# Kernel optimization log

Hardware: AMD Instinct MI355X
Metric: run time of the kernel (lower is better)

Reference implementation:

```python
import jax, jax.numpy as jnp
import numpy as np

CONF_THRES = 0.4
IOU_THRES = 0.45
MAX_WH = 4096.0   # class offset for class-aware NMS (agnostic=False)
MAX_DET = 300
B, N, NC = 8, 25200, 80


def setup_inputs() -> dict:
    key = jax.random.key(0)
    k1, k2, k3, k4, k5 = jax.random.split(key, 5)
    # realistic raw detector output: xywh in pixels, obj/cls scores in [0,1]
    xy = jax.random.uniform(k1, (B, N, 2), minval=0.0, maxval=608.0)
    wh = jax.random.uniform(k2, (B, N, 2), minval=4.0, maxval=96.0)
    obj = jax.random.uniform(k3, (B, N, 1))
    cls = jax.random.uniform(k4, (B, N, NC))
    prediction = jnp.concatenate([xy, wh, obj, cls], axis=-1)  # [B,N,85]
    logits = jax.random.normal(k5, (B, N, NC))
    return {"prediction": prediction, "logits": logits}


def _xywh2xyxy(b):
    cx, cy, w, h = b[..., 0], b[..., 1], b[..., 2], b[..., 3]
    return jnp.stack([cx - w / 2, cy - h / 2, cx + w / 2, cy + h / 2], axis=-1)


def _iou_one_vs_all(box, boxes):
    # box [4], boxes [N,4] -> IoU [N]
    lt = jnp.maximum(box[:2], boxes[:, :2])
    rb = jnp.minimum(box[2:], boxes[:, 2:])
    wh = jnp.clip(rb - lt, 0.0)
    inter = wh[:, 0] * wh[:, 1]
    a1 = (box[2] - box[0]) * (box[3] - box[1])
    a2 = (boxes[:, 2] - boxes[:, 0]) * (boxes[:, 3] - boxes[:, 1])
    return inter / (a1 + a2 - inter + 1e-9)


def _nms_image(pred, log_):
    # pred [N, 5+NC], log_ [N, NC]
    obj = pred[:, 4]
    scores_all = pred[:, 5:] * obj[:, None]          # x[:,5:] *= x[:,4:5]
    conf = scores_all.max(-1)                        # best-class conf
    cls = jnp.argmax(scores_all, -1)
    # obj-conf prefilter (xc mask) AND final conf filter, expressed as masking
    valid = (obj > CONF_THRES) & (conf > CONF_THRES)
    box = _xywh2xyxy(pred[:, :4])                    # [N,4]
    obox = box + (cls.astype(box.dtype) * MAX_WH)[:, None]  # class offset
    score0 = jnp.where(valid, conf, -1.0)

    def step(score_cur, _):
        idx = jnp.argmax(score_cur)
        keep = score_cur[idx] > 0.0
        iou = _iou_one_vs_all(obox[idx], obox)
        # suppress everything with IoU > thr (includes the picked box itself)
        new_score = jnp.where(keep & (iou > IOU_THRES), -1.0, score_cur)
        return new_score, (idx, keep)

    _, (idxs, keeps) = jax.lax.scan(step, score0, None, length=MAX_DET)
    m = keeps.astype(box.dtype)[:, None]
    dets = jnp.concatenate(
        [box[idxs], conf[idxs, None], cls[idxs, None].astype(box.dtype)], axis=-1
    ) * m                                            # [MAX_DET, 6], zero-padded
    return dets, log_[idxs] * m, keeps


def reference(prediction, logits):
    # returns (dets [B,300,6] = xyxy,conf,cls ; logits_sel [B,300,80] ; keep mask [B,300])
    return jax.vmap(_nms_image)(prediction, logits)
```

## Files before the change

kernel.cpp:

```cpp
#include <hip/hip_runtime.h>

#pragma clang fp contract(off)

#define NB 8
#define NN 25200
#define NCLS 80
#define NSTR 85
#define MAXDET 300
#define CONF_T 0.4f
#define IOU_T 0.45f
#define MAX_WH_C 4096.0f

#define NBIN 1024
#define BINSHIFT 14
#define BINBASE 0x3EC00000u
#define SELN 512
#define SORTN 2048
#define PREP_ROWS 64

typedef unsigned long long ull;

__device__ __forceinline__ float cand_score(const float* __restrict__ p) {
    float obj = p[4];
    float best = p[5] * obj;
    for (int j = 1; j < NCLS; ++j) {
        float s = p[5 + j] * obj;
        if (s > best) best = s;
    }
    return ((obj > CONF_T) && (best > CONF_T)) ? best : -1.0f;
}
__device__ __forceinline__ int cand_cls(const float* __restrict__ p) {
    float obj = p[4];
    float best = p[5] * obj; int bc = 0;
    for (int j = 1; j < NCLS; ++j) {
        float s = p[5 + j] * obj;
        if (s > best) { best = s; bc = j; }
    }
    return bc;
}
__device__ __forceinline__ bool iou_gt(float ax1, float ay1, float ax2, float ay2, float aarea,
                                       float bx1, float by1, float bx2, float by2, float barea) {
    float lx = fmaxf(ax1, bx1);
    float ly = fmaxf(ay1, by1);
    float rx = fminf(ax2, bx2);
    float ry = fminf(ay2, by2);
    float iw = fmaxf(rx - lx, 0.0f);
    float ih = fmaxf(ry - ly, 0.0f);
    float inter = iw * ih;
    float iou = inter / ((aarea + barea - inter) + 1e-9f);
    return iou > IOU_T;
}

__global__ __launch_bounds__(256) void prep_kernel(const float* __restrict__ pred,
                                                   float* __restrict__ score_ws,
                                                   int* __restrict__ cls_ws,
                                                   int write_cls) {
    __shared__ float st[PREP_ROWS * NSTR];
    const int R0 = blockIdx.x * PREP_ROWS;
    const float4* src = reinterpret_cast<const float4*>(pred + (size_t)R0 * NSTR);
    float4* dst4 = reinterpret_cast<float4*>(st);
    const int tid = threadIdx.x;
    for (int i = tid; i < PREP_ROWS * NSTR / 4; i += 256) dst4[i] = src[i];
    __syncthreads();

    int row = tid >> 2, part = tid & 3;
    const float* pr = st + row * NSTR;
    float obj = pr[4];
    float best = -1.0f; int bc = part * 20;
    const float* pc = pr + 5 + part * 20;
#pragma unroll
    for (int k = 0; k < 20; ++k) {
        float s = pc[k] * obj;
        if (s > best) { best = s; bc = part * 20 + k; }
    }
#pragma unroll
    for (int d = 1; d <= 2; d <<= 1) {
        float ob = __shfl_xor(best, d);
        int   oc = __shfl_xor(bc, d);
        if (ob > best || (ob == best && oc < bc)) { best = ob; bc = oc; }
    }
    if (part == 0) {
        int grow = R0 + row;
        bool valid = (obj > CONF_T) && (best > CONF_T);
        score_ws[grow] = valid ? best : -1.0f;
        if (write_cls) cls_ws[grow] = bc;
    }
}

__global__ __launch_bounds__(1024) void selimg_kernel(const float* __restrict__ pred,
                                                      const float* __restrict__ score_ws,
                                                      const int* __restrict__ cls_ws, int use_cls,
                                                      int* __restrict__ cnt_ws, int* __restrict__ total_ws,
                                                      ull* __restrict__ sel_key,
                                                      float* __restrict__ sel_x1, float* __restrict__ sel_y1,
                                                      float* __restrict__ sel_x2, float* __restrict__ sel_y2,
                                                      float* __restrict__ sel_area, float* __restrict__ sel_cls,
                                                      int* __restrict__ sel_idx) {
    __shared__ int s_hist[NBIN];
    __shared__ ull s_key[SELN];
    __shared__ int s_gidx[SELN];
    __shared__ int s_cnt, s_T, s_total;
    const int b = blockIdx.x;
    const int tid = threadIdx.x;
    const int lane = tid & 63;
    const int wid = tid >> 6;
    const float* predb = pred + (size_t)b * NN * NSTR;
    const float* sb = score_ws + (size_t)b * NN;

    s_hist[tid] = 0;
    if (tid == 0) s_cnt = 0;
    __syncthreads();
    for (int g = tid; g < NN; g += 1024) {
        float s = sb[g];
        if (s > 0.0f) {
            int bin = (int)((__float_as_uint(s) - BINBASE) >> BINSHIFT);
            atomicAdd(&s_hist[bin], 1);
        }
    }
    __syncthreads();
    if (wid == 0) {
        int acc = 0; int S[16];
#pragma unroll
        for (int k = 15; k >= 0; --k) { acc += s_hist[lane * 16 + k]; S[k] = acc; }
        int tot = acc;
        int incl = tot;
#pragma unroll
        for (int d = 1; d < 64; d <<= 1) {
            int v = __shfl_down(incl, d);
            if (lane + d < 64) incl += v;
        }
        int E = incl - tot;
        int Tl = NBIN;
#pragma unroll
        for (int k = 0; k < 16; ++k)
            if (Tl == NBIN && S[k] + E <= SELN) Tl = lane * 16 + k;
        int total0 = incl;
#pragma unroll
        for (int d = 1; d < 64; d <<= 1) {
            int o = __shfl_xor(Tl, d);
            if (o < Tl) Tl = o;
        }
        if (lane == 0) { s_T = Tl; s_total = total0; }
    }
    __syncthreads();
    int T = s_T;
    for (int g = tid; g < NN; g += 1024) {
        float s = sb[g];
        if (s > 0.0f) {
            int bin = (int)((__float_as_uint(s) - BINBASE) >> BINSHIFT);
            if (bin >= T) {
                int pos = atomicAdd(&s_cnt, 1);
                if (pos < SELN) {
                    s_key[pos] = ((ull)__float_as_uint(s) << 32)
                                 | (unsigned int)(0xFFFFFFFFu - (unsigned int)g);
                    s_gidx[pos] = g;
                }
            }
        }
    }
    __syncthreads();
    int cnt = s_cnt; if (cnt > SELN) cnt = SELN;

    if (tid < cnt) {
        int g = s_gidx[tid];
        const float* p = predb + (size_t)g * NSTR;
        float cx = p[0], cy = p[1], w = p[2], h = p[3];
        int c = use_cls ? cls_ws[(size_t)b * NN + g] : cand_cls(p);
        float off = (float)c * MAX_WH_C;
        float x1 = (cx - w * 0.5f) + off;
        float y1 = (cy - h * 0.5f) + off;
        float x2 = (cx + w * 0.5f) + off;
        float y2 = (cy + h * 0.5f) + off;
        int o = b * SELN + tid;
        sel_key[o] = s_key[tid];
        sel_x1[o] = x1; sel_y1[o] = y1; sel_x2[o] = x2; sel_y2[o] = y2;
        sel_area[o] = (x2 - x1) * (y2 - y1);
        sel_cls[o] = (float)c;
        sel_idx[o] = g;
    }
    if (tid == 0) { cnt_ws[b] = cnt; total_ws[b] = s_total; }
}

__global__ __launch_bounds__(256) void mask_kernel(const int* __restrict__ cnt_ws,
                                                   const ull* __restrict__ sel_key,
                                                   const float* __restrict__ sel_x1, const float* __restrict__ sel_y1,
                                                   const float* __restrict__ sel_x2, const float* __restrict__ sel_y2,
                                                   const float* __restrict__ sel_area,
                                                   ull* __restrict__ mask_ws) {
    __shared__ ull skey[SELN];
    __shared__ float ox1[SELN], oy1[SELN], ox2[SELN], oy2[SELN], oar[SELN];
    const int b = blockIdx.x >> 4;
    const int chunk = blockIdx.x & 15;
    const int tid = threadIdx.x;
    int cnt = cnt_ws[b]; if (cnt > SELN) cnt = SELN;
    for (int s = tid; s < SELN; s += 256) {
        if (s < cnt) {
            skey[s] = sel_key[b * SELN + s];
            ox1[s] = sel_x1[b * SELN + s]; oy1[s] = sel_y1[b * SELN + s];
            ox2[s] = sel_x2[b * SELN + s]; oy2[s] = sel_y2[b * SELN + s];
            oar[s] = sel_area[b * SELN + s];
        } else skey[s] = 0ull;
    }
    __syncthreads();
    int i = chunk * 32 + (tid & 31);
    int w = tid >> 5;
    if (i < cnt) {
        ull ki = skey[i];
        float ax1 = ox1[i], ay1 = oy1[i], ax2 = ox2[i], ay2 = oy2[i], aar = oar[i];
        ull m = 0ull;
        int jb = w << 6;
        int jend = cnt - jb; if (jend > 64) jend = 64;
        for (int t = 0; t < jend; ++t) {
            int j = jb + t;
            bool s = (skey[j] > ki) && iou_gt(ax1, ay1, ax2, ay2, aar,
                                             ox1[j], oy1[j], ox2[j], oy2[j], oar[j]);
            m |= (ull)s << t;
        }
        mask_ws[b * (8 * SELN) + w * SELN + i] = m;
    }
}

__global__ __launch_bounds__(1024) void resolve_kernel(
        const float* __restrict__ pred, const float* __restrict__ logits,
        const float* __restrict__ score_ws, const int* __restrict__ cls_ws, int use_cls,
        const int* __restrict__ cnt_ws, const int* __restrict__ total_ws,
        const ull* __restrict__ mask_ws, const ull* __restrict__ sel_key,
        const float* __restrict__ sel_x1, const float* __restrict__ sel_y1,
        const float* __restrict__ sel_x2, const float* __restrict__ sel_y2,
        const float* __restrict__ sel_area, const float* __restrict__ sel_cls,
        const int* __restrict__ sel_idx,
        float* __restrict__ out) {
    __shared__ ull s_m[8][SELN];
    __shared__ ull s_key[SELN];
    __shared__ ull s_kw[8];
    __shared__ ull s_minkey;
    __shared__ float s_x1[SELN], s_y1[SELN], s_x2[SELN], s_y2[SELN], s_ar[SELN], s_cl[SELN];
    __shared__ int s_ix[SELN];
    __shared__ float kx1[MAXDET], ky1[MAXDET], kx2[MAXDET], ky2[MAXDET], kar[MAXDET];
    __shared__ float ksc[MAXDET], kcl[MAXDET];
    __shared__ int kix[MAXDET];
    __shared__ int s_kc;

    const int b = blockIdx.x;
    const int tid = threadIdx.x;
    const int lane = tid & 63;
    const int wid = tid >> 6;
    const float* predb = pred + (size_t)b * NN * NSTR;
    const float* logb  = logits + (size_t)b * NN * NCLS;
    const float* sb    = score_ws + (size_t)b * NN;

    int cnt = cnt_ws[b]; if (cnt > SELN) cnt = SELN;

    for (int i = tid; i < 8 * SELN; i += 1024)
        (&s_m[0][0])[i] = mask_ws[b * (8 * SELN) + i];
    for (int s = tid; s < SELN; s += 1024) {
        if (s < cnt) {
            s_key[s] = sel_key[b * SELN + s];
            s_x1[s] = sel_x1[b * SELN + s]; s_y1[s] = sel_y1[b * SELN + s];
            s_x2[s] = sel_x2[b * SELN + s]; s_y2[s] = sel_y2[b * SELN + s];
            s_ar[s] = sel_area[b * SELN + s]; s_cl[s] = sel_cls[b * SELN + s];
            s_ix[s] = sel_idx[b * SELN + s];
        } else s_key[s] = 0ull;
    }
    __syncthreads();

    if (wid == 0) {
        ull mk = ~0ull;
#pragma unroll
        for (int r = 0; r < 8; ++r) {
            int i = (r << 6) + lane;
            if (i < cnt) { ull k = s_key[i]; if (k < mk) mk = k; }
        }
#pragma unroll
        for (int d = 32; d >= 1; d >>= 1) {
            ull o = __shfl_xor(mk, d);
            if (o < mk) mk = o;
        }
        if (lane == 0) s_minkey = mk;

        ull vm[8], kw[8];
#pragma unroll
        for (int r = 0; r < 8; ++r) {
            int lo = r << 6;
            vm[r] = (cnt >= lo + 64) ? ~0ull : (cnt > lo ? ((1ull << (cnt - lo)) - 1ull) : 0ull);
            kw[r] = vm[r];
        }
        for (int round = 0; round < SELN; ++round) {
            ull nw[8];
#pragma unroll
            for (int r = 0; r < 8; ++r) {
                int i = (r << 6) + lane;
                ull supp = 0ull;
#pragma unroll
                for (int w = 0; w < 8; ++w) supp |= kw[w] & s_m[w][i];
                nw[r] = __ballot((int)(supp == 0ull)) & vm[r];
            }
            bool changed = false;
#pragma unroll
            for (int r = 0; r < 8; ++r) { changed |= (nw[r] != kw[r]); kw[r] = nw[r]; }
            if (!changed) break;
        }
        int totkept = 0;
#pragma unroll
        for (int r = 0; r < 8; ++r) totkept += __popcll(kw[r]);
        if (lane == 0) s_kc = totkept < MAXDET ? totkept : MAXDET;
        if (lane < 8) s_kw[lane] = kw[lane];
    }
    __syncthreads();
    int kc = s_kc;

    if (tid < SELN) {
        bool kept = (s_kw[tid >> 6] >> (tid & 63)) & 1ull;
        if (!kept) s_key[tid] = 0ull;
    }
    __syncthreads();

    {
        int i = tid >> 1, half = tid & 1;
        ull k = s_key[i];
        int r = 0;
        if (k != 0ull) {
            int jb = half << 8;
            for (int jj = 0; jj < 256; ++jj) {
                ull kj = s_key[jb + jj];
                r += (int)(kj > k);
            }
        }
        r += __shfl_xor(r, 1);
        if (half == 0 && k != 0ull && r < MAXDET) {
            kx1[r] = s_x1[i]; ky1[r] = s_y1[i]; kx2[r] = s_x2[i]; ky2[r] = s_y2[i];
            kar[r] = s_ar[i]; ksc[r] = __uint_as_float((unsigned int)(k >> 32));
            kcl[r] = s_cl[i]; kix[r] = s_ix[i];
        }
    }
    __syncthreads();

    if (wid == 0 && kc < MAXDET && total_ws[b] > cnt) {
        ull prevkey = (cnt > 0) ? s_minkey : ~0ull;
        while (kc < MAXDET) {
            ull best = 0ull;
            for (int i0 = lane; i0 < NN; i0 += 64) {
                float s = sb[i0];
                if (s > 0.0f) {
                    ull key = ((ull)__float_as_uint(s) << 32)
                              | (unsigned int)(0xFFFFFFFFu - (unsigned int)i0);
                    if (key < prevkey && key > best) best = key;
                }
            }
#pragma unroll
            for (int d = 32; d >= 1; d >>= 1) {
                ull o = __shfl_xor(best, d);
                if (o > best) best = o;
            }
            if (best == 0ull) break;
            prevkey = best;
            int gi = (int)(0xFFFFFFFFu - (unsigned int)(best & 0xFFFFFFFFull));
            float sc = __uint_as_float((unsigned int)(best >> 32));
            const float* pp = predb + (size_t)gi * NSTR;
            float cx = pp[0], cy = pp[1], w = pp[2], h = pp[3];
            int c = use_cls ? cls_ws[(size_t)b * NN + gi] : cand_cls(pp);
            float off = (float)c * MAX_WH_C;
            float x1 = (cx - w * 0.5f) + off;
            float y1 = (cy - h * 0.5f) + off;
            float x2 = (cx + w * 0.5f) + off;
            float y2 = (cy + h * 0.5f) + off;
            float ar = (x2 - x1) * (y2 - y1);
            bool f = false;
            for (int t = lane; t < kc; t += 64)
                if (iou_gt(kx1[t], ky1[t], kx2[t], ky2[t], kar[t], x1, y1, x2, y2, ar)) f = true;
            if (!__any((int)f)) {
                if (lane == 0) {
                    kx1[kc] = x1; ky1[kc] = y1; kx2[kc] = x2; ky2[kc] = y2;
                    kar[kc] = ar; ksc[kc] = sc; kcl[kc] = (float)c; kix[kc] = gi;
                }
                kc++;
            }
        }
        if (lane == 0) s_kc = kc;
    }
    __syncthreads();
    kc = s_kc;

    if (tid < MAXDET) {
        int t = tid;
        float o0 = 0, o1 = 0, o2 = 0, o3 = 0, o4 = 0, o5 = 0;
        if (t < kc) {
            int idx = kix[t];
            const float* pp = predb + (size_t)idx * NSTR;
            float cx = pp[0], cy = pp[1], w = pp[2], h = pp[3];
            o0 = cx - w * 0.5f; o1 = cy - h * 0.5f;
            o2 = cx + w * 0.5f; o3 = cy + h * 0.5f;
            o4 = ksc[t];        o5 = kcl[t];
        }
        float* dd = out + (size_t)b * (MAXDET * 6) + (size_t)t * 6;
        dd[0] = o0; dd[1] = o1; dd[2] = o2; dd[3] = o3; dd[4] = o4; dd[5] = o5;
        out[(size_t)NB * MAXDET * 6 + (size_t)NB * MAXDET * NCLS + (size_t)b * MAXDET + t] =
            (t < kc) ? 1.0f : 0.0f;
    }
    float* lbase = out + (size_t)NB * MAXDET * 6 + (size_t)b * (MAXDET * NCLS);
    for (int t = wid; t < MAXDET; t += 16) {
        float* dst = lbase + (size_t)t * NCLS;
        if (t < kc) {
            const float* src = logb + (size_t)kix[t] * NCLS;
            for (int c = lane; c < NCLS; c += 64) dst[c] = src[c];
        } else {
            for (int c = lane; c < NCLS; c += 64) dst[c] = 0.0f;
        }
    }
}

__global__ __launch_bounds__(1024) void fallback_kernel(const float* __restrict__ pred,
                                                        const float* __restrict__ logits,
                                                        float* __restrict__ out) {
    __shared__ ull s_keys[SORTN];
    __shared__ float sel_x1[SORTN], sel_y1[SORTN], sel_x2[SORTN], sel_y2[SORTN];
    __shared__ float sel_area[SORTN], sel_cls[SORTN];
    __shared__ int   sel_idx[SORTN];
    __shared__ float kx1[MAXDET], ky1[MAXDET], kx2[MAXDET], ky2[MAXDET], karea[MAXDET];
    __shared__ float kscore[MAXDET], kcls[MAXDET];
    __shared__ int   kidx[MAXDET];
    __shared__ int   s_hist[NBIN];
    __shared__ int   s_suppk[64];
    __shared__ unsigned int s_supmask[64][2];
    __shared__ int   s_kc, s_T, s_cnt;

    const int b = blockIdx.x;
    const int tid = threadIdx.x;
    const int lane = tid & 63;
    const int wid = tid >> 6;
    const float* predb = pred + (size_t)b * NN * NSTR;
    const float* logb  = logits + (size_t)b * NN * NCLS;

    int kc_total = 0;
    int prevT = NBIN;

    while (kc_total < MAXDET && prevT > 0) {
        s_hist[tid] = 0;
        if (tid == 0) { s_cnt = 0; s_T = NBIN; }
        __syncthreads();
        for (int i = tid; i < NN; i += 1024) {
            float s = cand_score(predb + (size_t)i * NSTR);
            if (s > 0.0f) {
                int bin = (int)((__float_as_uint(s) - BINBASE) >> BINSHIFT);
                if (bin < prevT) atomicAdd(&s_hist[bin], 1);
            }
        }
        __syncthreads();
        for (int d = 1; d < NBIN; d <<= 1) {
            int v = s_hist[tid] + ((tid + d < NBIN) ? s_hist[tid + d] : 0);
            __syncthreads();
            s_hist[tid] = v;
            __syncthreads();
        }
        if (s_hist[tid] <= SORTN) atomicMin(&s_T, tid);
        __syncthreads();
        int T = s_T;
        int rem_total = s_hist[0];
        if (T >= prevT) {
            if (rem_total == 0) { prevT = 0; break; }
            T = prevT - 1;
        }
        __syncthreads();
        for (int i = tid; i < NN; i += 1024) {
            float s = cand_score(predb + (size_t)i * NSTR);
            if (s > 0.0f) {
                int bin = (int)((__float_as_uint(s) - BINBASE) >> BINSHIFT);
                if (bin >= T && bin < prevT) {
                    int pos = atomicAdd(&s_cnt, 1);
                    if (pos < SORTN)
                        s_keys[pos] = ((ull)__float_as_uint(s) << 32)
                                      | (unsigned int)(0xFFFFFFFFu - (unsigned int)i);
                }
            }
        }
        __syncthreads();
        int cnt = s_cnt; if (cnt > SORTN) cnt = SORTN;
        int npow = 64; while (npow < cnt) npow <<= 1;
        for (int i = cnt + tid; i < npow; i += 1024) s_keys[i] = 0ull;
        __syncthreads();
        for (int k = 2; k <= npow; k <<= 1) {
            for (int j = k >> 1; j > 0; j >>= 1) {
                for (int idx = tid; idx < npow; idx += 1024) {
                    int p = idx ^ j;
                    if (p > idx) {
                        ull a = s_keys[idx], c = s_keys[p];
                        bool desc = ((idx & k) == 0);
                        if (desc ? (a < c) : (a > c)) { s_keys[idx] = c; s_keys[p] = a; }
                    }
                }
                __syncthreads();
            }
        }
        for (int t = tid; t < cnt; t += 1024) {
            ull key = s_keys[t];
            int i = (int)(0xFFFFFFFFu - (unsigned int)(key & 0xFFFFFFFFull));
            const float* p = predb + (size_t)i * NSTR;
            float cx = p[0], cy = p[1], w = p[2], h = p[3];
            int c = cand_cls(p);
            float off = (float)c * MAX_WH_C;
            float x1 = (cx - w * 0.5f) + off;
            float y1 = (cy - h * 0.5f) + off;
            float x2 = (cx + w * 0.5f) + off;
            float y2 = (cy + h * 0.5f) + off;
            sel_x1[t] = x1; sel_y1[t] = y1; sel_x2[t] = x2; sel_y2[t] = y2;
            sel_area[t] = (x2 - x1) * (y2 - y1);
            sel_cls[t] = (float)c;
            sel_idx[t] = i;
        }
        __syncthreads();
        int nb2 = (cnt + 63) >> 6;
        for (int batch = 0; batch < nb2; ++batch) {
            int kcb = kc_total;
            if (kcb >= MAXDET) break;
            if (tid < 64) { s_suppk[tid] = 0; s_supmask[tid][0] = 0u; s_supmask[tid][1] = 0u; }
            __syncthreads();
            int cloc = tid >> 4, ch = tid & 15;
            int gi = batch * 64 + cloc;
            bool validc = gi < cnt;
            float ax1 = 0, ay1 = 0, ax2 = 0, ay2 = 0, aar = 0;
            if (validc) {
                ax1 = sel_x1[gi]; ay1 = sel_y1[gi];
                ax2 = sel_x2[gi]; ay2 = sel_y2[gi]; aar = sel_area[gi];
            }
            bool flag = false;
            if (validc) {
                for (int t = ch; t < kcb; t += 16) {
                    if (iou_gt(kx1[t], ky1[t], kx2[t], ky2[t], karea[t],
                               ax1, ay1, ax2, ay2, aar)) flag = true;
                }
            }
            ull bal = __ballot((int)flag);
            if ((lane & 15) == 0) {
                unsigned int sub = (unsigned int)((bal >> (lane & 48)) & 0xFFFFull);
                s_suppk[cloc] = (sub != 0u);
            }
            unsigned int mbits = 0;
            if (validc) {
                for (int jj = 0; jj < 4; ++jj) {
                    int j = (ch << 2) + jj;
                    int gj = batch * 64 + j;
                    if (j > cloc && gj < cnt) {
                        if (iou_gt(ax1, ay1, ax2, ay2, aar,
                                   sel_x1[gj], sel_y1[gj], sel_x2[gj], sel_y2[gj], sel_area[gj]))
                            mbits |= 1u << (j & 31);
                    }
                }
            }
            if (mbits) atomicOr(&s_supmask[cloc][(ch >> 3) & 1], mbits);
            __syncthreads();
            if (wid == 0) {
                ull mask = ((ull)s_supmask[lane][1] << 32) | s_supmask[lane][0];
                bool validj = (batch * 64 + lane) < cnt;
                ull rem = __ballot((int)(validj && (s_suppk[lane] == 0)));
                ull keepbits = 0;
                int kcount = kcb;
                while (rem && kcount < MAXDET) {
                    int i = __builtin_ctzll(rem);
                    rem &= rem - 1;
                    keepbits |= 1ull << i;
                    ++kcount;
                    ull mi = __shfl(mask, i);
                    rem &= ~mi;
                }
                if ((keepbits >> lane) & 1ull) {
                    int pos = kcb + __popcll(keepbits & ((1ull << lane) - 1ull));
                    int g2 = batch * 64 + lane;
                    kx1[pos] = sel_x1[g2]; ky1[pos] = sel_y1[g2];
                    kx2[pos] = sel_x2[g2]; ky2[pos] = sel_y2[g2];
                    karea[pos] = sel_area[g2];
                    kcls[pos] = sel_cls[g2]; kidx[pos] = sel_idx[g2];
                    kscore[pos] = __uint_as_float((unsigned int)(s_keys[g2] >> 32));
                }
                if (lane == 0) s_kc = kcount;
            }
            __syncthreads();
            kc_total = s_kc;
            __syncthreads();
        }
        prevT = T;
    }

    __syncthreads();
    int kc = kc_total;
    if (tid < MAXDET) {
        int t = tid;
        float o0 = 0, o1 = 0, o2 = 0, o3 = 0, o4 = 0, o5 = 0;
        if (t < kc) {
            int idx = kidx[t];
            const float* pp = predb + (size_t)idx * NSTR;
            float cx = pp[0], cy = pp[1], w = pp[2], h = pp[3];
            o0 = cx - w * 0.5f; o1 = cy - h * 0.5f;
            o2 = cx + w * 0.5f; o3 = cy + h * 0.5f;
            o4 = kscore[t];     o5 = kcls[t];
        }
        float* dd = out + (size_t)b * (MAXDET * 6) + (size_t)t * 6;
        dd[0] = o0; dd[1] = o1; dd[2] = o2; dd[3] = o3; dd[4] = o4; dd[5] = o5;
        out[(size_t)NB * MAXDET * 6 + (size_t)NB * MAXDET * NCLS + (size_t)b * MAXDET + t] =
            (t < kc) ? 1.0f : 0.0f;
    }
    float* lbase = out + (size_t)NB * MAXDET * 6 + (size_t)b * (MAXDET * NCLS);
    for (int t = wid; t < MAXDET; t += 16) {
        float* dst = lbase + (size_t)t * NCLS;
        if (t < kc) {
            const float* src = logb + (size_t)kidx[t] * NCLS;
            for (int c = lane; c < NCLS; c += 64) dst[c] = src[c];
        } else {
            for (int c = lane; c < NCLS; c += 64) dst[c] = 0.0f;
        }
    }
}

extern "C" void kernel_launch(void* const* d_in, const int* in_sizes, int n_in,
                              void* d_out, int out_size, void* d_ws, size_t ws_size,
                              hipStream_t stream) {
    const float* pred   = (const float*)d_in[0];
    const float* logits = (const float*)d_in[1];
    float* out = (float*)d_out;

    const size_t off_mask  = 0;
    const size_t off_key   = 262144;
    const size_t off_flt   = 294912;
    const size_t off_ix    = off_flt + 6 * 16384;
    const size_t off_score = off_ix + 16384;
    const size_t off_cnt   = off_score + 806400;
    const size_t off_tot   = off_cnt + 32;
    const size_t need_base = off_tot + 32;
    const size_t off_cls   = need_base;
    const size_t need_full = off_cls + 806400;

    if (d_ws == nullptr || ws_size < need_base) {
        fallback_kernel<<<NB, 1024, 0, stream>>>(pred, logits, out);
        return;
    }

    char* ws = (char*)d_ws;
    ull*   mask_ws  = (ull*)(ws + off_mask);
    ull*   sel_key  = (ull*)(ws + off_key);
    float* sel_x1   = (float*)(ws + off_flt);
    float* sel_y1   = sel_x1 + NB * SELN;
    float* sel_x2   = sel_y1 + NB * SELN;
    float* sel_y2   = sel_x2 + NB * SELN;
    float* sel_area = sel_y2 + NB * SELN;
    float* sel_cls  = sel_area + NB * SELN;
    int*   sel_idx  = (int*)(ws + off_ix);
    float* score_ws = (float*)(ws + off_score);
    int*   cnt_ws   = (int*)(ws + off_cnt);
    int*   total_ws = (int*)(ws + off_tot);
    int*   cls_ws   = (int*)(ws + off_cls);
    int use_cls = (ws_size >= need_full) ? 1 : 0;

    prep_kernel<<<(NB * NN) / PREP_ROWS, 256, 0, stream>>>(pred, score_ws, cls_ws, use_cls);
    selimg_kernel<<<NB, 1024, 0, stream>>>(pred, score_ws, cls_ws, use_cls,
                                           cnt_ws, total_ws, sel_key,
                                           sel_x1, sel_y1, sel_x2, sel_y2,
                                           sel_area, sel_cls, sel_idx);
    mask_kernel<<<NB * 16, 256, 0, stream>>>(cnt_ws, sel_key,
                                             sel_x1, sel_y1, sel_x2, sel_y2, sel_area, mask_ws);
    resolve_kernel<<<NB, 1024, 0, stream>>>(pred, logits, score_ws, cls_ws, use_cls,
                                            cnt_ws, total_ws, mask_ws, sel_key,
                                            sel_x1, sel_y1, sel_x2, sel_y2,
                                            sel_area, sel_cls, sel_idx, out);
}
```

Before: 75.94 us.

## Fuse candidate selection and IoU mask build into one kernel per image quarter

Adds a fused kernel that runs histogram thresholding, a deterministic prefix-scan compaction of top candidates, box decoding and the pairwise IoU suppression mask, with four blocks per image each computing a quarter of the mask rows. This removes one kernel launch and the global round trip of the selected boxes between selection and mask stages, and replaces the atomic-append compaction with an ordered scan. The trade-off is that each of the four blocks redundantly repeats the histogram and selection passes over the image's scores. The old two-kernel path remains as a fallback when the workspace is too small.

```diff
diff --git a/kernel.cpp b/kernel.cpp
--- a/kernel.cpp
+++ b/kernel.cpp
@@ -87,9 +87,158 @@
     }
 }
 
+__global__ __launch_bounds__(1024) void selmask3_kernel(const float* __restrict__ pred,
+        const float* __restrict__ score_ws, const int* __restrict__ cls_ws,
+        int* __restrict__ cnt_ws, int* __restrict__ total_ws,
+        ull* __restrict__ sel_key,
+        float* __restrict__ sel_x1, float* __restrict__ sel_y1,
+        float* __restrict__ sel_x2, float* __restrict__ sel_y2,
+        float* __restrict__ sel_area, float* __restrict__ sel_cls,
+        int* __restrict__ sel_idx,
+        ull* __restrict__ mask_ws) {
+    __shared__ int s_hist[NBIN];
+    __shared__ int s_c[1024], s_off[1024];
+    __shared__ ull s_key[SELN];
+    __shared__ int s_gidx[SELN];
+    __shared__ float m_x1[SELN], m_y1[SELN], m_x2[SELN], m_y2[SELN], m_ar[SELN], m_cl[SELN];
+    __shared__ int sT, sTot, sSel;
+
+    const int b = blockIdx.x >> 2;
+    const int quarter = blockIdx.x & 3;
+    const int tid = threadIdx.x;
+    const int lane = tid & 63;
+    const float* sb = score_ws + (size_t)b * NN;
+    const float* predb = pred + (size_t)b * NN * NSTR;
+
+    s_hist[tid] = 0;
+    __syncthreads();
+    for (int g = tid; g < NN; g += 1024) {
+        float s = sb[g];
+        if (s > 0.0f) {
+            int bin = (int)((__float_as_uint(s) - BINBASE) >> BINSHIFT);
+            atomicAdd(&s_hist[bin], 1);
+        }
+    }
+    __syncthreads();
+
+    if (tid < 64) {
+        int acc = 0; int S[16];
+#pragma unroll
+        for (int k = 15; k >= 0; --k) { acc += s_hist[lane * 16 + k]; S[k] = acc; }
+        int tot = acc;
+        int incl = tot;
+#pragma unroll
+        for (int d = 1; d < 64; d <<= 1) {
+            int v = __shfl_down(incl, d);
+            if (lane + d < 64) incl += v;
+        }
+        int E = incl - tot;
+        int Tl = NBIN;
+#pragma unroll
+        for (int k = 0; k < 16; ++k)
+            if (Tl == NBIN && S[k] + E <= SELN) Tl = lane * 16 + k;
+        int total0 = incl;
+#pragma unroll
+        for (int d = 1; d < 64; d <<= 1) {
+            int o = __shfl_xor(Tl, d);
+            if (o < Tl) Tl = o;
+        }
+        if (lane == 0) { sT = Tl; sTot = total0; }
+    }
+    __syncthreads();
+    int T = sT;
+
+    int c = 0;
+    for (int g = tid; g < NN; g += 1024) {
+        float s = sb[g];
+        if (s > 0.0f && (int)((__float_as_uint(s) - BINBASE) >> BINSHIFT) >= T) ++c;
+    }
+    s_c[tid] = c;
+    __syncthreads();
+    if (tid < 64) {
+        int base = tid << 4;
+        int pre[16]; int run = 0;
+#pragma unroll
+        for (int k = 0; k < 16; ++k) { pre[k] = run; run += s_c[base + k]; }
+        int inc = run;
+#pragma unroll
+        for (int d = 1; d < 64; d <<= 1) {
+            int v = __shfl_up(inc, d);
+            if (lane >= d) inc += v;
+        }
+        int ex = inc - run;
+#pragma unroll
+        for (int k = 0; k < 16; ++k) s_off[base + k] = ex + pre[k];
+        if (lane == 63) sSel = ex + run;
+    }
+    __syncthreads();
+    {
+        int r = s_off[tid];
+        for (int g = tid; g < NN; g += 1024) {
+            float s = sb[g];
+            if (s > 0.0f && (int)((__float_as_uint(s) - BINBASE) >> BINSHIFT) >= T) {
+                if (r < SELN) {
+                    s_key[r] = ((ull)__float_as_uint(s) << 32)
+                               | (unsigned int)(0xFFFFFFFFu - (unsigned int)g);
+                    s_gidx[r] = g;
+                }
+                ++r;
+            }
+        }
+    }
+    __syncthreads();
+    int cnt = sSel; if (cnt > SELN) cnt = SELN;
+
+    if (tid < cnt) {
+        int g = s_gidx[tid];
+        const float* p = predb + (size_t)g * NSTR;
+        float cx = p[0], cy = p[1], w = p[2], h = p[3];
+        int cc = cls_ws[(size_t)b * NN + g];
+        float off = (float)cc * MAX_WH_C;
+        float x1 = (cx - w * 0.5f) + off;
+        float y1 = (cy - h * 0.5f) + off;
+        float x2 = (cx + w * 0.5f) + off;
+        float y2 = (cy + h * 0.5f) + off;
+        m_x1[tid] = x1; m_y1[tid] = y1; m_x2[tid] = x2; m_y2[tid] = y2;
+        m_ar[tid] = (x2 - x1) * (y2 - y1);
+        m_cl[tid] = (float)cc;
+    }
+    __syncthreads();
+
+    {
+        int w = tid >> 7;
+        int i = quarter * 128 + (tid & 127);
+        if (i < cnt) {
+            ull ki = s_key[i];
+            float ax1 = m_x1[i], ay1 = m_y1[i], ax2 = m_x2[i], ay2 = m_y2[i], aar = m_ar[i];
+            ull m = 0ull;
+            int jb = w << 6;
+            int jend = cnt - jb; if (jend > 64) jend = 64;
+            for (int t = 0; t < jend; ++t) {
+                int j = jb + t;
+                bool sres = (s_key[j] > ki) && iou_gt(ax1, ay1, ax2, ay2, aar,
+                                                     m_x1[j], m_y1[j], m_x2[j], m_y2[j], m_ar[j]);
+                m |= (ull)sres << t;
+            }
+            mask_ws[b * (8 * SELN) + w * SELN + i] = m;
+        }
+    }
+
+    if (quarter == 0) {
+        for (int s = tid; s < cnt; s += 1024) {
+            int o = b * SELN + s;
+            sel_key[o] = s_key[s];
+            sel_x1[o] = m_x1[s]; sel_y1[o] = m_y1[s];
+            sel_x2[o] = m_x2[s]; sel_y2[o] = m_y2[s];
+            sel_area[o] = m_ar[s]; sel_cls[o] = m_cl[s];
+            sel_idx[o] = s_gidx[s];
+        }
+        if (tid == 0) { cnt_ws[b] = cnt; total_ws[b] = sTot; }
+    }
+}
+
 __global__ __launch_bounds__(1024) void selimg_kernel(const float* __restrict__ pred,
                                                       const float* __restrict__ score_ws,
-                                                      const int* __restrict__ cls_ws, int use_cls,
                                                       int* __restrict__ cnt_ws, int* __restrict__ total_ws,
                                                       ull* __restrict__ sel_key,
                                                       float* __restrict__ sel_x1, float* __restrict__ sel_y1,
@@ -165,7 +314,7 @@
         int g = s_gidx[tid];
         const float* p = predb + (size_t)g * NSTR;
         float cx = p[0], cy = p[1], w = p[2], h = p[3];
-        int c = use_cls ? cls_ws[(size_t)b * NN + g] : cand_cls(p);
+        int c = cand_cls(p);
         float off = (float)c * MAX_WH_C;
         float x1 = (cx - w * 0.5f) + off;
         float y1 = (cy - h * 0.5f) + off;
@@ -650,12 +799,18 @@
     int use_cls = (ws_size >= need_full) ? 1 : 0;
 
     prep_kernel<<<(NB * NN) / PREP_ROWS, 256, 0, stream>>>(pred, score_ws, cls_ws, use_cls);
-    selimg_kernel<<<NB, 1024, 0, stream>>>(pred, score_ws, cls_ws, use_cls,
-                                           cnt_ws, total_ws, sel_key,
-                                           sel_x1, sel_y1, sel_x2, sel_y2,
-                                           sel_area, sel_cls, sel_idx);
-    mask_kernel<<<NB * 16, 256, 0, stream>>>(cnt_ws, sel_key,
-                                             sel_x1, sel_y1, sel_x2, sel_y2, sel_area, mask_ws);
+    if (use_cls) {
+        selmask3_kernel<<<NB * 4, 1024, 0, stream>>>(pred, score_ws, cls_ws,
+                                                     cnt_ws, total_ws, sel_key,
+                                                     sel_x1, sel_y1, sel_x2, sel_y2,
+                                                     sel_area, sel_cls, sel_idx, mask_ws);
+    } else {
+        selimg_kernel<<<NB, 1024, 0, stream>>>(pred, score_ws, cnt_ws, total_ws, sel_key,
+                                               sel_x1, sel_y1, sel_x2, sel_y2,
+                                               sel_area, sel_cls, sel_idx);
+        mask_kernel<<<NB * 16, 256, 0, stream>>>(cnt_ws, sel_key,
+                                                 sel_x1, sel_y1, sel_x2, sel_y2, sel_area, mask_ws);
+    }
     resolve_kernel<<<NB, 1024, 0, stream>>>(pred, logits, score_ws, cls_ws, use_cls,
                                             cnt_ws, total_ws, mask_ws, sel_key,
                                             sel_x1, sel_y1, sel_x2, sel_y2,
```

Result: slower. 79.44 us (+4.6%).
